# Kernel optimization log

Hardware: AMD Instinct MI355X
Metric: run time of the kernel (lower is better)

## Reference

```python
import jax, jax.numpy as jnp
import numpy as np

N = 100000   # nodes
E = 1600000  # edges
D = 128      # input_dim == hidden_dim
OUT = 64     # output_dim
G = 64       # graphs in batch
L = 4        # GIN layers = num_layers - 1
BN_EPS = 1e-5


def setup_inputs() -> dict:
    key = jax.random.key(0)
    ks = jax.random.split(key, 16)
    inp = {
        "h": jax.random.normal(ks[0], (N, D), dtype=jnp.float32),
        "efeat": jnp.zeros((1,), dtype=jnp.float32),
        "src": jax.random.randint(ks[1], (E,), 0, N, dtype=jnp.int32),
        "dst": jax.random.randint(ks[2], (E,), 0, N, dtype=jnp.int32),
        "graph_id": jnp.sort(jax.random.randint(ks[3], (N,), 0, G, dtype=jnp.int32)),
        # learnable eps per GIN layer (init 0, as GINConv(init_eps=0))
        "eps": jnp.zeros((L,), dtype=jnp.float32),
        # 2-layer MLP per GIN layer
        "mlp_W1": jax.random.normal(ks[4], (L, D, D), dtype=jnp.float32) / np.sqrt(D),
        "mlp_b1": jnp.zeros((L, D), dtype=jnp.float32),
        "mlp_W2": jax.random.normal(ks[5], (L, D, D), dtype=jnp.float32) / np.sqrt(D),
        "mlp_b2": jnp.zeros((L, D), dtype=jnp.float32),
        # BN inside MLP (after first linear)
        "mlp_bn_g": jnp.ones((L, D), dtype=jnp.float32),
        "mlp_bn_b": jnp.zeros((L, D), dtype=jnp.float32),
        # BN of ApplyNodeFunc
        "apply_bn_g": jnp.ones((L, D), dtype=jnp.float32),
        "apply_bn_b": jnp.zeros((L, D), dtype=jnp.float32),
        # outer per-layer BN in UnsupervisedGIN
        "outer_bn_g": jnp.ones((L, D), dtype=jnp.float32),
        "outer_bn_b": jnp.zeros((L, D), dtype=jnp.float32),
        # prediction heads: layer 0 on input (D) + L heads on hidden (D)
        "pred_W": jax.random.normal(ks[6], (L + 1, D, OUT), dtype=jnp.float32) / np.sqrt(D),
        "pred_b": jnp.zeros((L + 1, OUT), dtype=jnp.float32),
    }
    return inp


def _bn(x, g, b):
    # train-mode BatchNorm1d over node axis
    m = x.mean(axis=0)
    v = x.var(axis=0)
    return (x - m) * jax.lax.rsqrt(v + BN_EPS) * g + b


def reference(h, efeat, src, dst, graph_id, eps,
              mlp_W1, mlp_b1, mlp_W2, mlp_b2,
              mlp_bn_g, mlp_bn_b, apply_bn_g, apply_bn_b,
              outer_bn_g, outer_bn_b, pred_W, pred_b):
    hidden_rep = [h]
    for i in range(L):
        # GINConv, neighbor_pooling = sum: aggregate src features into dst
        agg = jax.ops.segment_sum(h[src], dst, num_segments=N)  # [N, D]
        x = (1.0 + eps[i]) * h + agg
        # ApplyNodeFunc: MLP(2 layers) -> BN -> ReLU
        z = jax.nn.relu(_bn(x @ mlp_W1[i] + mlp_b1[i], mlp_bn_g[i], mlp_bn_b[i]))
        z = z @ mlp_W2[i] + mlp_b2[i]
        z = jax.nn.relu(_bn(z, apply_bn_g[i], apply_bn_b[i]))
        # outer BN + ReLU
        h = jax.nn.relu(_bn(z, outer_bn_g[i], outer_bn_b[i]))
        hidden_rep.append(h)

    # SumPooling per layer + prediction heads (dropout = identity at eval)
    pooled = [jax.ops.segment_sum(hh, graph_id, num_segments=G) for hh in hidden_rep]
    score = sum(p @ pred_W[i] + pred_b[i] for i, p in enumerate(pooled))  # [G, OUT]
    return (score, tuple(pooled[1:]))
```

## Files before the change

### kernel.cpp

```cpp
#include <hip/hip_runtime.h>

constexpr int D   = 128;
constexpr int G   = 64;
constexpr int OUT = 64;
constexpr int L   = 4;
#define BN_EPS 1e-5f

constexpr int BSH    = 9;
constexpr int BNODES = 1 << BSH;
constexpr int SC_CHUNK = 8192;
constexpr int SRC_BITS = 17;
constexpr int SRC_MASK = (1 << SRC_BITS) - 1;

typedef __attribute__((ext_vector_type(8))) short bf16x8;
typedef __attribute__((ext_vector_type(4))) short short4v;
typedef __attribute__((ext_vector_type(4))) float f32x4;
typedef unsigned short u16;

__device__ inline u16 f2bf(float f) {
    union { float f; unsigned u; } x; x.f = f;
    unsigned r = x.u + 0x7FFF + ((x.u >> 16) & 1);
    return (u16)(r >> 16);
}
__device__ inline float bf2f(u16 u) {
    union { unsigned u; float f; } x; x.u = ((unsigned)u) << 16;
    return x.f;
}

__global__ __launch_bounds__(256) void bucket_hist(const int* __restrict__ dst,
                                                   int* __restrict__ bktCnt,
                                                   int nE, int numB) {
    __shared__ int h[4096];
    const int tid = threadIdx.x;
    for (int i = tid; i < numB; i += 256) h[i] = 0;
    __syncthreads();
    const int stride = gridDim.x * 256;
    for (int e = blockIdx.x * 256 + tid; e < nE; e += stride)
        atomicAdd(&h[dst[e] >> BSH], 1);
    __syncthreads();
    for (int i = tid; i < numB; i += 256)
        if (h[i]) atomicAdd(&bktCnt[i], h[i]);
}

__global__ __launch_bounds__(256) void scan_buckets(const int* __restrict__ bktCnt,
                                                    int* __restrict__ bktOff,
                                                    int* __restrict__ bktCur,
                                                    int numB, int total) {
    __shared__ int sm[256];
    const int tid = threadIdx.x;
    int v[4];
    int s = 0;
#pragma unroll
    for (int j = 0; j < 4; ++j) {
        int i = tid * 4 + j;
        v[j] = (i < numB) ? bktCnt[i] : 0;
        s += v[j];
    }
    sm[tid] = s;
    __syncthreads();
    for (int off = 1; off < 256; off <<= 1) {
        int t = (tid >= off) ? sm[tid - off] : 0;
        __syncthreads();
        sm[tid] += t;
        __syncthreads();
    }
    int run = sm[tid] - s;
#pragma unroll
    for (int j = 0; j < 4; ++j) {
        int i = tid * 4 + j;
        if (i < numB) { bktOff[i] = run; bktCur[i] = run; }
        run += v[j];
    }
    if (tid == 0) bktOff[numB] = total;
}

__global__ __launch_bounds__(256) void bucket_scatter(const int* __restrict__ src,
                                                      const int* __restrict__ dst,
                                                      int* __restrict__ bktCur,
                                                      int* __restrict__ sorted,
                                                      int nE, int numB) {
    __shared__ int h[1024];
    __shared__ int base[1024];
    const int tid = threadIdx.x;
    const int lo = blockIdx.x * SC_CHUNK;
    const int hi = min(lo + SC_CHUNK, nE);
    for (int i = tid; i < numB; i += 256) h[i] = 0;
    __syncthreads();
    for (int e = lo + tid; e < hi; e += 256)
        atomicAdd(&h[dst[e] >> BSH], 1);
    __syncthreads();
    for (int i = tid; i < numB; i += 256) {
        int c = h[i];
        base[i] = c ? atomicAdd(&bktCur[i], c) : 0;
        h[i] = 0;
    }
    __syncthreads();
    for (int e = lo + tid; e < hi; e += 256) {
        int d = dst[e];
        int b = d >> BSH;
        int pos = base[b] + atomicAdd(&h[b], 1);
        sorted[pos] = src[e] | ((d & (BNODES - 1)) << SRC_BITS);
    }
}

__global__ __launch_bounds__(256) void bucket_deg(const int* __restrict__ sorted,
                                                  const int* __restrict__ bktOff,
                                                  int* __restrict__ deg, int nN) {
    __shared__ int h[BNODES];
    const int tid = threadIdx.x;
    const int b = blockIdx.x;
    for (int j = tid; j < BNODES; j += 256) h[j] = 0;
    __syncthreads();
    const int lo = bktOff[b], hi = bktOff[b + 1];
    for (int i = lo + tid; i < hi; i += 256)
        atomicAdd(&h[(sorted[i] >> SRC_BITS) & (BNODES - 1)], 1);
    __syncthreads();
    const int node0 = b << BSH;
    for (int j = tid; j < BNODES; j += 256) {
        int n = node0 + j;
        if (n < nN) deg[n] = h[j];
    }
}

__global__ __launch_bounds__(256) void csr_fill2(const int* __restrict__ sorted,
                                                 const int* __restrict__ bktOff,
                                                 const int* __restrict__ rowptr,
                                                 int* __restrict__ esrc, int nN) {
    __shared__ int cur[BNODES];
    const int tid = threadIdx.x;
    const int b = blockIdx.x;
    const int node0 = b << BSH;
    for (int j = tid; j < BNODES; j += 256) {
        int n = node0 + j;
        cur[j] = (n < nN) ? rowptr[n] : 0;
    }
    __syncthreads();
    const int lo = bktOff[b], hi = bktOff[b + 1];
    for (int i = lo + tid; i < hi; i += 256) {
        int p = sorted[i];
        int pos = atomicAdd(&cur[(p >> SRC_BITS) & (BNODES - 1)], 1);
        esrc[pos] = p & SRC_MASK;
    }
}

constexpr int SCAN_B = 256;
constexpr int SCAN_E = 8;
constexpr int SCAN_CHUNK = SCAN_B * SCAN_E;

__global__ __launch_bounds__(SCAN_B) void scan_pass1(const int* __restrict__ deg,
                                                     int* __restrict__ rowptr,
                                                     int* __restrict__ bsum, int n) {
    __shared__ int sm[SCAN_B];
    const int tid = threadIdx.x;
    const int base = blockIdx.x * SCAN_CHUNK + tid * SCAN_E;
    int v[SCAN_E];
    int s = 0;
#pragma unroll
    for (int j = 0; j < SCAN_E; ++j) {
        v[j] = (base + j < n) ? deg[base + j] : 0;
        s += v[j];
    }
    sm[tid] = s;
    __syncthreads();
    for (int off = 1; off < SCAN_B; off <<= 1) {
        int t = (tid >= off) ? sm[tid - off] : 0;
        __syncthreads();
        sm[tid] += t;
        __syncthreads();
    }
    int run = sm[tid] - s;
#pragma unroll
    for (int j = 0; j < SCAN_E; ++j) {
        if (base + j < n) rowptr[base + j] = run;
        run += v[j];
    }
    if (tid == SCAN_B - 1) bsum[blockIdx.x] = sm[SCAN_B - 1];
}

__global__ void scan_pass2(int* __restrict__ bsum, int nb) {
    if (threadIdx.x == 0 && blockIdx.x == 0) {
        int t = 0;
        for (int i = 0; i < nb; ++i) {
            int s = bsum[i];
            bsum[i] = t;
            t += s;
        }
    }
}

__global__ __launch_bounds__(SCAN_B) void scan_pass3(int* __restrict__ rowptr,
                                                     const int* __restrict__ bsum,
                                                     int n, int total) {
    const int add = bsum[blockIdx.x];
    const int base = blockIdx.x * SCAN_CHUNK + threadIdx.x * SCAN_E;
#pragma unroll
    for (int j = 0; j < SCAN_E; ++j)
        if (base + j < n) rowptr[base + j] += add;
    if (blockIdx.x == 0 && threadIdx.x == 0) rowptr[n] = total;
}

__global__ void prep_weights(const float* __restrict__ W1, const float* __restrict__ W2,
                             u16* __restrict__ Wt) {
    const int m = blockIdx.x;
    const float* W = (m < L) ? (W1 + (size_t)m * D * D) : (W2 + (size_t)(m - L) * D * D);
    u16* o = Wt + (size_t)m * D * D;
    for (int e = threadIdx.x * 4; e < D * D; e += 256 * 4) {
        float4 v = *reinterpret_cast<const float4*>(W + e);
        int k = e >> 7, c = e & 127;
        o[(c + 0) * D + k] = f2bf(v.x);
        o[(c + 1) * D + k] = f2bf(v.y);
        o[(c + 2) * D + k] = f2bf(v.z);
        o[(c + 3) * D + k] = f2bf(v.w);
    }
}

__global__ __launch_bounds__(256) void convert_pool(const float* __restrict__ h, const int* __restrict__ gid,
                                                    u16* __restrict__ hbf, float* __restrict__ pooled,
                                                    int nRows) {
    const int tid = threadIdx.x;
    const int c = tid & 127;
    const int rsub = tid >> 7;
    const long long row0 = (long long)blockIdx.x * 64;
    float acc = 0.f;
    int cur = -1;
    for (int r = rsub; r < 64; r += 2) {
        long long row = row0 + r;
        if (row >= nRows) break;
        float v = h[row * D + c];
        hbf[row * D + c] = f2bf(v);
        int g = gid[row];
        if (g != cur) {
            if (cur >= 0) atomicAdd(&pooled[(long long)cur * D + c], acc);
            cur = g;
            acc = 0.f;
        }
        acc += v;
    }
    if (cur >= 0) atomicAdd(&pooled[(long long)cur * D + c], acc);
}

__global__ __launch_bounds__(256) void agg_gather(const u16* __restrict__ hbf,
                                                  const int* __restrict__ rowptr,
                                                  const int* __restrict__ esrc,
                                                  const float* __restrict__ epsP,
                                                  u16* __restrict__ xbf, int nRows) {
    const int r = blockIdx.x * 16 + (threadIdx.x >> 4);
    if (r >= nRows) return;
    const int c = (threadIdx.x & 15) * 8;
    const int beg = rowptr[r], end = rowptr[r + 1];
    const float ep = 1.0f + epsP[0];
    bf16x8 a = *reinterpret_cast<const bf16x8*>(hbf + (size_t)r * D + c);
    float acc[8];
#pragma unroll
    for (int j = 0; j < 8; ++j) acc[j] = ep * bf2f((u16)a[j]);

    int e = beg;
    for (; e + 8 <= end; e += 8) {
        bf16x8 v[8];
#pragma unroll
        for (int q = 0; q < 8; ++q) {
            int s = esrc[e + q];
            v[q] = *reinterpret_cast<const bf16x8*>(hbf + (size_t)s * D + c);
        }
#pragma unroll
        for (int j = 0; j < 8; ++j) {
            float t0 = (bf2f((u16)v[0][j]) + bf2f((u16)v[1][j])) + (bf2f((u16)v[2][j]) + bf2f((u16)v[3][j]));
            float t1 = (bf2f((u16)v[4][j]) + bf2f((u16)v[5][j])) + (bf2f((u16)v[6][j]) + bf2f((u16)v[7][j]));
            acc[j] += t0 + t1;
        }
    }
    for (; e + 4 <= end; e += 4) {
        bf16x8 v[4];
#pragma unroll
        for (int q = 0; q < 4; ++q) {
            int s = esrc[e + q];
            v[q] = *reinterpret_cast<const bf16x8*>(hbf + (size_t)s * D + c);
        }
#pragma unroll
        for (int j = 0; j < 8; ++j)
            acc[j] += (bf2f((u16)v[0][j]) + bf2f((u16)v[1][j])) + (bf2f((u16)v[2][j]) + bf2f((u16)v[3][j]));
    }
    for (; e < end; ++e) {
        int s = esrc[e];
        bf16x8 v = *reinterpret_cast<const bf16x8*>(hbf + (size_t)s * D + c);
#pragma unroll
        for (int j = 0; j < 8; ++j) acc[j] += bf2f((u16)v[j]);
    }
    bf16x8 o;
#pragma unroll
    for (int j = 0; j < 8; ++j) o[j] = (short)f2bf(acc[j]);
    *reinterpret_cast<bf16x8*>(xbf + (size_t)r * D + c) = o;
}

constexpr int CSTRIDE = D + 8;

template <int MODE>
__global__ __launch_bounds__(256) void gemm_mfma(
    const u16* __restrict__ A, const u16* __restrict__ Wt, const float* __restrict__ bias,
    const float* __restrict__ pSum, const float* __restrict__ pSq,
    const float* __restrict__ bng, const float* __restrict__ bnb, float invN,
    u16* __restrict__ outP, float* __restrict__ gsum, float* __restrict__ gsq,
    int nRows) {
    __shared__ u16 wLx[D * CSTRIDE];
    __shared__ float redS[D], redQ[D];
    __shared__ float scL[D], shL[D];

    const int tid = threadIdx.x;
    const int row0 = blockIdx.x * 128;
    const int lane = tid & 63;
    const int wv = tid >> 6;
    const int wrow = wv * 32;
    const int lr = lane & 15;
    const int lb = lane >> 4;

    bf16x8 aR[2][4];
    bool valid[2];
#pragma unroll
    for (int m = 0; m < 2; ++m) {
        int row = row0 + wrow + m * 16 + lr;
        valid[m] = row < nRows;
        const u16* p = A + (size_t)(valid[m] ? row : (nRows - 1)) * D + lb * 8;
#pragma unroll
        for (int kk = 0; kk < 4; ++kk)
            aR[m][kk] = *reinterpret_cast<const bf16x8*>(p + kk * 32);
    }

    for (int o = tid * 8; o < D * D; o += 2048) {
        bf16x8 v = *reinterpret_cast<const bf16x8*>(Wt + o);
        int byte = o * 2, r = byte >> 8;
        *reinterpret_cast<bf16x8*>((char*)wLx + (byte ^ ((r & 7) << 4))) = v;
    }
    if (tid < D) {
        redS[tid] = 0.f; redQ[tid] = 0.f;
        if (MODE == 1) {
            float m = pSum[tid] * invN;
            float v = pSq[tid] * invN - m * m;
            float sc = bng[tid] * rsqrtf(v + BN_EPS);
            scL[tid] = sc;
            shL[tid] = bnb[tid] - m * sc;
        }
    }
    __syncthreads();

    if (MODE == 1) {
#pragma unroll
        for (int m = 0; m < 2; ++m)
#pragma unroll
            for (int kk = 0; kk < 4; ++kk)
#pragma unroll
                for (int j = 0; j < 8; ++j) {
                    int c = kk * 32 + lb * 8 + j;
                    float t = fmaxf(bf2f((u16)aR[m][kk][j]) * scL[c] + shL[c], 0.f);
                    aR[m][kk][j] = (short)f2bf(t);
                }
    }
#pragma unroll
    for (int m = 0; m < 2; ++m)
        if (!valid[m])
#pragma unroll
            for (int kk = 0; kk < 4; ++kk) aR[m][kk] = bf16x8{};

    f32x4 acc[2][8] = {};
#pragma unroll
    for (int kk = 0; kk < 4; ++kk) {
#pragma unroll
        for (int n = 0; n < 8; ++n) {
            int cr = n * 16 + lr;
            int byte = cr * 256 + kk * 64 + lb * 16;
            bf16x8 bF = *reinterpret_cast<const bf16x8*>((char*)wLx + (byte ^ ((cr & 7) << 4)));
            acc[0][n] = __builtin_amdgcn_mfma_f32_16x16x32_bf16(aR[0][kk], bF, acc[0][n], 0, 0, 0);
            acc[1][n] = __builtin_amdgcn_mfma_f32_16x16x32_bf16(aR[1][kk], bF, acc[1][n], 0, 0, 0);
        }
    }
    __syncthreads();

    float ls[8], lq[8];
#pragma unroll
    for (int n = 0; n < 8; ++n) { ls[n] = 0.f; lq[n] = 0.f; }
#pragma unroll
    for (int n = 0; n < 8; ++n) {
        int col = n * 16 + lr;
        float bv = bias[col];
#pragma unroll
        for (int m = 0; m < 2; ++m) {
#pragma unroll
            for (int j = 0; j < 4; ++j) {
                int rloc = wrow + m * 16 + lb * 4 + j;
                float o = acc[m][n][j] + bv;
                wLx[rloc * CSTRIDE + col] = f2bf(o);
                if (row0 + rloc < nRows) { ls[n] += o; lq[n] += o * o; }
            }
        }
    }
#pragma unroll
    for (int n = 0; n < 8; ++n) {
        float s = ls[n], q = lq[n];
        s += __shfl_xor(s, 16); q += __shfl_xor(q, 16);
        s += __shfl_xor(s, 32); q += __shfl_xor(q, 32);
        if (lb == 0) {
            atomicAdd(&redS[n * 16 + lr], s);
            atomicAdd(&redQ[n * 16 + lr], q);
        }
    }
    __syncthreads();

    {
        int rloc = tid >> 1;
        int row = row0 + rloc;
        if (row < nRows) {
            const int c0 = (tid & 1) * 64;
            const u16* srcL = wLx + rloc * CSTRIDE + c0;
            u16* dstG = outP + (size_t)row * D + c0;
#pragma unroll
            for (int q = 0; q < 8; ++q)
                *reinterpret_cast<bf16x8*>(dstG + q * 8) =
                    *reinterpret_cast<const bf16x8*>(srcL + q * 8);
        }
    }
    if (tid < D) {
        atomicAdd(&gsum[tid], redS[tid]);
        atomicAdd(&gsq[tid], redQ[tid]);
    }
}

__global__ __launch_bounds__(256) void relu_bn_stats(const u16* __restrict__ z,
                                                     const float* __restrict__ pSum, const float* __restrict__ pSq,
                                                     const float* __restrict__ bng, const float* __restrict__ bnb,
                                                     float invN,
                                                     float* __restrict__ gsum, float* __restrict__ gsq,
                                                     long long n8) {
    __shared__ float redS[D], redQ[D];
    const int tid = threadIdx.x;
    if (tid < D) { redS[tid] = 0.f; redQ[tid] = 0.f; }
    __syncthreads();
    const int c = (tid & 15) * 8;
    float sc[8], sh[8];
#pragma unroll
    for (int j = 0; j < 8; ++j) {
        float m = pSum[c + j] * invN;
        float v = pSq[c + j] * invN - m * m;
        float s = bng[c + j] * rsqrtf(v + BN_EPS);
        sc[j] = s;
        sh[j] = bnb[c + j] - m * s;
    }
    const long long stride = (long long)gridDim.x * blockDim.x;
    float ls[8] = {}, lq[8] = {};
    for (long long i = (long long)blockIdx.x * blockDim.x + tid; i < n8; i += stride) {
        bf16x8 v = *reinterpret_cast<const bf16x8*>(z + i * 8);
#pragma unroll
        for (int j = 0; j < 8; ++j) {
            float t = fmaxf(bf2f((u16)v[j]) * sc[j] + sh[j], 0.f);
            ls[j] += t; lq[j] += t * t;
        }
    }
#pragma unroll
    for (int j = 0; j < 8; ++j) {
        atomicAdd(&redS[c + j], ls[j]);
        atomicAdd(&redQ[c + j], lq[j]);
    }
    __syncthreads();
    if (tid < D) {
        atomicAdd(&gsum[tid], redS[tid]);
        atomicAdd(&gsq[tid], redQ[tid]);
    }
}

__global__ __launch_bounds__(256) void final_apply_pool(
    const u16* __restrict__ z, const int* __restrict__ gid,
    const float* __restrict__ p1S, const float* __restrict__ p1Q,
    const float* __restrict__ g2, const float* __restrict__ b2v,
    const float* __restrict__ p2S, const float* __restrict__ p2Q,
    const float* __restrict__ g3, const float* __restrict__ b3v,
    float invN, u16* __restrict__ hbf, float* __restrict__ pooled, int nRows) {
    const int tid = threadIdx.x;
    const int c = tid & 127;
    const int rsub = tid >> 7;
    const long long row0 = (long long)blockIdx.x * 64;

    float m = p1S[c] * invN;
    float va = p1Q[c] * invN - m * m;
    float a2 = g2[c] * rsqrtf(va + BN_EPS);
    float f2v = b2v[c] - m * a2;
    m = p2S[c] * invN;
    va = p2Q[c] * invN - m * m;
    float a3 = g3[c] * rsqrtf(va + BN_EPS);
    float f3v = b3v[c] - m * a3;

    float acc = 0.f;
    int cur = -1;
    for (int r = rsub; r < 64; r += 2) {
        long long row = row0 + r;
        if (row >= nRows) break;
        float v = bf2f(z[row * D + c]);
        v = fmaxf(fmaxf(v * a2 + f2v, 0.f) * a3 + f3v, 0.f);
        hbf[row * D + c] = f2bf(v);
        int g = gid[row];
        if (g != cur) {
            if (cur >= 0) atomicAdd(&pooled[(long long)cur * D + c], acc);
            cur = g;
            acc = 0.f;
        }
        acc += v;
    }
    if (cur >= 0) atomicAdd(&pooled[(long long)cur * D + c], acc);
}

__global__ __launch_bounds__(256) void pred_heads(const float* __restrict__ pooled0,
                                                  const float* __restrict__ pooledL,
                                                  const float* __restrict__ pW,
                                                  const float* __restrict__ pb,
                                                  float* __restrict__ score) {
    __shared__ float red[256];
    __shared__ float pL[D];
    const int g = blockIdx.x;
    const int o = threadIdx.x & 63;
    const int ks = threadIdx.x >> 6;
    float acc = 0.f;
    for (int i = 0; i <= L; ++i) {
        const float* p = (i == 0) ? (pooled0 + (size_t)g * D)
                                  : (pooledL + (size_t)(i - 1) * G * D + (size_t)g * D);
        if (threadIdx.x < D) pL[threadIdx.x] = p[threadIdx.x];
        __syncthreads();
        const float* w = pW + (size_t)i * D * OUT + (size_t)ks * 32 * OUT + o;
        float s = 0.f;
#pragma unroll
        for (int kk = 0; kk < 32; ++kk)
            s += pL[ks * 32 + kk] * w[kk * OUT];
        acc += s;
        if (ks == 0) acc += pb[i * OUT + o];
        __syncthreads();
    }
    red[threadIdx.x] = acc;
    __syncthreads();
    if (ks == 0)
        score[(size_t)g * OUT + o] = red[o] + red[64 + o] + red[128 + o] + red[192 + o];
}

extern "C" void kernel_launch(void* const* d_in, const int* in_sizes, int n_in,
                              void* d_out, int out_size, void* d_ws, size_t ws_size,
                              hipStream_t stream) {
    const float* h0  = (const float*)d_in[0];
    const int*   src = (const int*)d_in[2];
    const int*   dst = (const int*)d_in[3];
    const int*   gid = (const int*)d_in[4];
    const float* eps = (const float*)d_in[5];
    const float* W1  = (const float*)d_in[6];
    const float* b1  = (const float*)d_in[7];
    const float* W2  = (const float*)d_in[8];
    const float* b2  = (const float*)d_in[9];
    const float* bn1g = (const float*)d_in[10];
    const float* bn1b = (const float*)d_in[11];
    const float* bn2g = (const float*)d_in[12];
    const float* bn2b = (const float*)d_in[13];
    const float* bn3g = (const float*)d_in[14];
    const float* bn3b = (const float*)d_in[15];
    const float* pW  = (const float*)d_in[16];
    const float* pb  = (const float*)d_in[17];

    const int N = in_sizes[0] / D;
    const int E = in_sizes[2];
    const size_t nd = (size_t)N * D;
    const int numB = (N + BNODES - 1) >> BSH;

    u16*   hbf  = (u16*)d_ws;
    u16*   xbf  = hbf + nd;
    u16*   Wt   = xbf + nd;
    float* stats = (float*)(Wt + (size_t)2 * L * D * D);
    float* pooled0 = stats + (size_t)L * 3 * 2 * D;
    int*   bktCnt = (int*)(pooled0 + (size_t)G * D);
    int*   bktOff = bktCnt + 4096;
    int*   bktCur = bktOff + 4096;
    int*   deg    = bktCur + 4096;
    int*   rowptr = deg + N;
    int*   esrc   = rowptr + (N + 1);
    int*   bsum   = esrc + E;
    int*   sorted = bsum + 4096;

    float* score = (float*)d_out;
    float* pooledOut = score + G * OUT;

    auto S = [&](int i, int j) { return stats + (size_t)(i * 3 + j) * 2 * D; };
    auto Q = [&](int i, int j) { return stats + (size_t)(i * 3 + j) * 2 * D + D; };

    const int nb = (N + SCAN_CHUNK - 1) / SCAN_CHUNK;
    const int sgrid = (E + SC_CHUNK - 1) / SC_CHUNK;
    const int hgrid = (E + 2047) / 2048;
    const int poolGrid = (N + 63) / 64;
    const int ggrid = (N + 127) / 128;
    const int agrid = (N + 15) / 16;
    const long long n8 = (long long)N * (D / 8);
    const float invN = 1.0f / (float)N;

    const size_t zeroBytes = ((size_t)L * 3 * 2 * D + (size_t)G * D) * sizeof(float) + 4096 * sizeof(int);
    hipMemsetAsync(stats, 0, zeroBytes, stream);
    hipMemsetAsync(d_out, 0, (size_t)out_size * sizeof(float), stream);

    bucket_hist<<<hgrid, 256, 0, stream>>>(dst, bktCnt, E, numB);
    prep_weights<<<2 * L, 256, 0, stream>>>(W1, W2, Wt);
    scan_buckets<<<1, 256, 0, stream>>>(bktCnt, bktOff, bktCur, numB, E);
    bucket_scatter<<<sgrid, 256, 0, stream>>>(src, dst, bktCur, sorted, E, numB);
    bucket_deg<<<numB, 256, 0, stream>>>(sorted, bktOff, deg, N);
    scan_pass1<<<nb, SCAN_B, 0, stream>>>(deg, rowptr, bsum, N);
    scan_pass2<<<1, 64, 0, stream>>>(bsum, nb);
    scan_pass3<<<nb, SCAN_B, 0, stream>>>(rowptr, bsum, N, E);
    csr_fill2<<<numB, 256, 0, stream>>>(sorted, bktOff, rowptr, esrc, N);

    convert_pool<<<poolGrid, 256, 0, stream>>>(h0, gid, hbf, pooled0, N);

    for (int i = 0; i < L; ++i) {
        agg_gather<<<agrid, 256, 0, stream>>>(hbf, rowptr, esrc, eps + i, xbf, N);

        gemm_mfma<2><<<ggrid, 256, 0, stream>>>(
            xbf, Wt + (size_t)i * D * D, b1 + (size_t)i * D,
            nullptr, nullptr, nullptr, nullptr, invN,
            xbf, S(i, 0), Q(i, 0), N);

        gemm_mfma<1><<<ggrid, 256, 0, stream>>>(
            xbf, Wt + (size_t)(L + i) * D * D, b2 + (size_t)i * D,
            S(i, 0), Q(i, 0), bn1g + (size_t)i * D, bn1b + (size_t)i * D, invN,
            xbf, S(i, 1), Q(i, 1), N);

        relu_bn_stats<<<1024, 256, 0, stream>>>(
            xbf, S(i, 1), Q(i, 1), bn2g + (size_t)i * D, bn2b + (size_t)i * D, invN,
            S(i, 2), Q(i, 2), n8);

        final_apply_pool<<<poolGrid, 256, 0, stream>>>(
            xbf, gid,
            S(i, 1), Q(i, 1), bn2g + (size_t)i * D, bn2b + (size_t)i * D,
            S(i, 2), Q(i, 2), bn3g + (size_t)i * D, bn3b + (size_t)i * D,
            invN, hbf, pooledOut + (size_t)i * G * D, N);
    }

    pred_heads<<<G, 256, 0, stream>>>(pooled0, pooledOut, pW, pb, score);
}
```

Before: 875.6 us.

## Fuse neighbor aggregation into first MLP GEMM via shared-memory tile

Merges the CSR gather-sum kernel with the first MFMA GEMM. Each 128-row block aggregates its rows into a swizzled LDS tile, then multiplies by W1 and accumulates BN statistics. This removes the bf16 write and re-read of the aggregated features and one launch per layer. In exchange, each block spends a long irregular gather phase before its GEMM, and the 256-thread blocks with large LDS may hide gather latency less well than the old 16-rows-per-block kernel.

```diff
diff --git a/kernel.cpp b/kernel.cpp
--- a/kernel.cpp
+++ b/kernel.cpp
@@ -239,60 +239,151 @@
     if (cur >= 0) atomicAdd(&pooled[(long long)cur * D + c], acc);
 }
 
-__global__ __launch_bounds__(256) void agg_gather(const u16* __restrict__ hbf,
-                                                  const int* __restrict__ rowptr,
-                                                  const int* __restrict__ esrc,
-                                                  const float* __restrict__ epsP,
-                                                  u16* __restrict__ xbf, int nRows) {
-    const int r = blockIdx.x * 16 + (threadIdx.x >> 4);
-    if (r >= nRows) return;
-    const int c = (threadIdx.x & 15) * 8;
-    const int beg = rowptr[r], end = rowptr[r + 1];
+constexpr int CSTRIDE = D + 8;
+
+__global__ __launch_bounds__(256) void agg_gemm1(
+    const u16* __restrict__ hbf, const int* __restrict__ rowptr,
+    const int* __restrict__ esrc, const float* __restrict__ epsP,
+    const u16* __restrict__ Wt, const float* __restrict__ bias,
+    u16* __restrict__ outP, float* __restrict__ gsum, float* __restrict__ gsq,
+    int nRows) {
+    __shared__ u16 aLx[D * CSTRIDE];
+    __shared__ float redS[D], redQ[D];
+
+    const int tid = threadIdx.x;
+    const int row0 = blockIdx.x * 128;
     const float ep = 1.0f + epsP[0];
-    bf16x8 a = *reinterpret_cast<const bf16x8*>(hbf + (size_t)r * D + c);
-    float acc[8];
-#pragma unroll
-    for (int j = 0; j < 8; ++j) acc[j] = ep * bf2f((u16)a[j]);
-
-    int e = beg;
-    for (; e + 8 <= end; e += 8) {
-        bf16x8 v[8];
-#pragma unroll
-        for (int q = 0; q < 8; ++q) {
-            int s = esrc[e + q];
-            v[q] = *reinterpret_cast<const bf16x8*>(hbf + (size_t)s * D + c);
-        }
-#pragma unroll
-        for (int j = 0; j < 8; ++j) {
-            float t0 = (bf2f((u16)v[0][j]) + bf2f((u16)v[1][j])) + (bf2f((u16)v[2][j]) + bf2f((u16)v[3][j]));
-            float t1 = (bf2f((u16)v[4][j]) + bf2f((u16)v[5][j])) + (bf2f((u16)v[6][j]) + bf2f((u16)v[7][j]));
-            acc[j] += t0 + t1;
-        }
-    }
-    for (; e + 4 <= end; e += 4) {
-        bf16x8 v[4];
-#pragma unroll
-        for (int q = 0; q < 4; ++q) {
-            int s = esrc[e + q];
-            v[q] = *reinterpret_cast<const bf16x8*>(hbf + (size_t)s * D + c);
-        }
-#pragma unroll
-        for (int j = 0; j < 8; ++j)
-            acc[j] += (bf2f((u16)v[0][j]) + bf2f((u16)v[1][j])) + (bf2f((u16)v[2][j]) + bf2f((u16)v[3][j]));
-    }
-    for (; e < end; ++e) {
-        int s = esrc[e];
-        bf16x8 v = *reinterpret_cast<const bf16x8*>(hbf + (size_t)s * D + c);
-#pragma unroll
-        for (int j = 0; j < 8; ++j) acc[j] += bf2f((u16)v[j]);
-    }
-    bf16x8 o;
-#pragma unroll
-    for (int j = 0; j < 8; ++j) o[j] = (short)f2bf(acc[j]);
-    *reinterpret_cast<bf16x8*>(xbf + (size_t)r * D + c) = o;
-}
-
-constexpr int CSTRIDE = D + 8;
+
+    if (tid < D) { redS[tid] = 0.f; redQ[tid] = 0.f; }
+
+    const int grp = tid >> 4;
+    const int c = (tid & 15) * 8;
+    for (int k = 0; k < 8; ++k) {
+        const int rloc = grp + k * 16;
+        const int byte = rloc * 256 + c * 2;
+        bf16x8* dstL = reinterpret_cast<bf16x8*>((char*)aLx + (byte ^ ((rloc & 7) << 4)));
+        const long long row = row0 + rloc;
+        if (row < nRows) {
+            const int beg = rowptr[row], end = rowptr[row + 1];
+            bf16x8 a = *reinterpret_cast<const bf16x8*>(hbf + row * D + c);
+            float acc[8];
+#pragma unroll
+            for (int j = 0; j < 8; ++j) acc[j] = ep * bf2f((u16)a[j]);
+            int e = beg;
+            for (; e + 8 <= end; e += 8) {
+                bf16x8 v[8];
+#pragma unroll
+                for (int q = 0; q < 8; ++q) {
+                    int s = esrc[e + q];
+                    v[q] = *reinterpret_cast<const bf16x8*>(hbf + (size_t)s * D + c);
+                }
+#pragma unroll
+                for (int j = 0; j < 8; ++j) {
+                    float t0 = (bf2f((u16)v[0][j]) + bf2f((u16)v[1][j])) + (bf2f((u16)v[2][j]) + bf2f((u16)v[3][j]));
+                    float t1 = (bf2f((u16)v[4][j]) + bf2f((u16)v[5][j])) + (bf2f((u16)v[6][j]) + bf2f((u16)v[7][j]));
+                    acc[j] += t0 + t1;
+                }
+            }
+            for (; e + 4 <= end; e += 4) {
+                bf16x8 v[4];
+#pragma unroll
+                for (int q = 0; q < 4; ++q) {
+                    int s = esrc[e + q];
+                    v[q] = *reinterpret_cast<const bf16x8*>(hbf + (size_t)s * D + c);
+                }
+#pragma unroll
+                for (int j = 0; j < 8; ++j)
+                    acc[j] += (bf2f((u16)v[0][j]) + bf2f((u16)v[1][j])) + (bf2f((u16)v[2][j]) + bf2f((u16)v[3][j]));
+            }
+            for (; e < end; ++e) {
+                int s = esrc[e];
+                bf16x8 v = *reinterpret_cast<const bf16x8*>(hbf + (size_t)s * D + c);
+#pragma unroll
+                for (int j = 0; j < 8; ++j) acc[j] += bf2f((u16)v[j]);
+            }
+            bf16x8 o;
+#pragma unroll
+            for (int j = 0; j < 8; ++j) o[j] = (short)f2bf(acc[j]);
+            *dstL = o;
+        } else {
+            *dstL = bf16x8{};
+        }
+    }
+    __syncthreads();
+
+    const int lane = tid & 63;
+    const int wv = tid >> 6;
+    const int wrow = wv * 32;
+    const int lr = lane & 15;
+    const int lb = lane >> 4;
+
+    f32x4 acc[2][8] = {};
+#pragma unroll
+    for (int kk = 0; kk < 4; ++kk) {
+        bf16x8 aF[2];
+#pragma unroll
+        for (int m = 0; m < 2; ++m) {
+            int r = wrow + m * 16 + lr;
+            int byte = r * 256 + kk * 64 + lb * 16;
+            aF[m] = *reinterpret_cast<const bf16x8*>((char*)aLx + (byte ^ ((r & 7) << 4)));
+        }
+#pragma unroll
+        for (int n = 0; n < 8; ++n) {
+            int cr = n * 16 + lr;
+            bf16x8 bF = *reinterpret_cast<const bf16x8*>(Wt + (size_t)cr * D + kk * 32 + lb * 8);
+            acc[0][n] = __builtin_amdgcn_mfma_f32_16x16x32_bf16(aF[0], bF, acc[0][n], 0, 0, 0);
+            acc[1][n] = __builtin_amdgcn_mfma_f32_16x16x32_bf16(aF[1], bF, acc[1][n], 0, 0, 0);
+        }
+    }
+    __syncthreads();
+
+    float ls[8], lq[8];
+#pragma unroll
+    for (int n = 0; n < 8; ++n) { ls[n] = 0.f; lq[n] = 0.f; }
+#pragma unroll
+    for (int n = 0; n < 8; ++n) {
+        int col = n * 16 + lr;
+        float bv = bias[col];
+#pragma unroll
+        for (int m = 0; m < 2; ++m) {
+#pragma unroll
+            for (int j = 0; j < 4; ++j) {
+                int rloc = wrow + m * 16 + lb * 4 + j;
+                float o = acc[m][n][j] + bv;
+                aLx[rloc * CSTRIDE + col] = f2bf(o);
+                if (row0 + rloc < nRows) { ls[n] += o; lq[n] += o * o; }
+            }
+        }
+    }
+#pragma unroll
+    for (int n = 0; n < 8; ++n) {
+        float s = ls[n], q = lq[n];
+        s += __shfl_xor(s, 16); q += __shfl_xor(q, 16);
+        s += __shfl_xor(s, 32); q += __shfl_xor(q, 32);
+        if (lb == 0) {
+            atomicAdd(&redS[n * 16 + lr], s);
+            atomicAdd(&redQ[n * 16 + lr], q);
+        }
+    }
+    __syncthreads();
+    {
+        int rloc = tid >> 1;
+        int row = row0 + rloc;
+        if (row < nRows) {
+            const int c0 = (tid & 1) * 64;
+            const u16* srcL = aLx + rloc * CSTRIDE + c0;
+            u16* dstG = outP + (size_t)row * D + c0;
+#pragma unroll
+            for (int q = 0; q < 8; ++q)
+                *reinterpret_cast<bf16x8*>(dstG + q * 8) =
+                    *reinterpret_cast<const bf16x8*>(srcL + q * 8);
+        }
+    }
+    if (tid < D) {
+        atomicAdd(&gsum[tid], redS[tid]);
+        atomicAdd(&gsq[tid], redQ[tid]);
+    }
+}
 
 template <int MODE>
 __global__ __launch_bounds__(256) void gemm_mfma(
@@ -587,7 +678,6 @@
     const int hgrid = (E + 2047) / 2048;
     const int poolGrid = (N + 63) / 64;
     const int ggrid = (N + 127) / 128;
-    const int agrid = (N + 15) / 16;
     const long long n8 = (long long)N * (D / 8);
     const float invN = 1.0f / (float)N;
 
@@ -608,11 +698,9 @@
     convert_pool<<<poolGrid, 256, 0, stream>>>(h0, gid, hbf, pooled0, N);
 
     for (int i = 0; i < L; ++i) {
-        agg_gather<<<agrid, 256, 0, stream>>>(hbf, rowptr, esrc, eps + i, xbf, N);
-
-        gemm_mfma<2><<<ggrid, 256, 0, stream>>>(
-            xbf, Wt + (size_t)i * D * D, b1 + (size_t)i * D,
-            nullptr, nullptr, nullptr, nullptr, invN,
+        agg_gemm1<<<ggrid, 256, 0, stream>>>(
+            hbf, rowptr, esrc, eps + i,
+            Wt + (size_t)i * D * D, b1 + (size_t)i * D,
             xbf, S(i, 0), Q(i, 0), N);
 
         gemm_mfma<1><<<ggrid, 256, 0, stream>>>(
```

Measured after the change: 963.0 us. 10.0% more time.
